# Optimization experiments

Hardware: AMD Instinct MI355X
Metric: run time of the kernel (lower is better)

Reference implementation:

```python
import jax, jax.numpy as jnp
import numpy as np

B, N, NE = 4, 10000, 100000
D, S, H, T = 128, 64, 4, 128      # enc_dim, enc_s_dim, n_head, n_token
NS = D + S                        # GNN node_size = 192
EPS = 1e-5


def linear(x, w, b):
    return x @ w.T + b


def layer_norm(x, g, b):
    m = jnp.mean(x, -1, keepdims=True)
    v = jnp.mean((x - m) ** 2, -1, keepdims=True)
    return (x - m) * jax.lax.rsqrt(v + EPS) * g + b


def mha(q, k, v, wqkv, bqkv, wo, bo):
    # torch nn.MultiheadAttention, batch_first=True
    d = q.shape[-1]; hd = d // H
    wq, wk, wv = jnp.split(wqkv, 3, 0)
    bq, bk, bv = jnp.split(bqkv, 3, 0)
    def proj(x, w, bb):
        Bx, L, _ = x.shape
        return (x @ w.T + bb).reshape(Bx, L, H, hd)
    qh, kh, vh = proj(q, wq, bq), proj(k, wk, bk), proj(v, wv, bv)
    scores = jnp.einsum('bqhd,bkhd->bhqk', qh, kh) / jnp.sqrt(jnp.asarray(hd, q.dtype))
    att = jax.nn.softmax(scores, axis=-1)
    o = jnp.einsum('bhqk,bkhd->bqhd', att, vh).reshape(q.shape[0], q.shape[1], d)
    return o @ wo.T + bo


def smean(vals, idx, n):
    # scatter_mean over one batch element: vals (ne,f), idx (ne,)
    s = jax.ops.segment_sum(vals, idx, num_segments=n)
    c = jax.ops.segment_sum(jnp.ones(idx.shape, vals.dtype), idx, num_segments=n)
    return s / jnp.maximum(c, 1.0)[:, None]

_smean_b = jax.vmap(smean, in_axes=(0, 0, None))
_gather_b = jax.vmap(lambda v, i: v[i])


def setup_inputs():
    key = jax.random.key(0)
    ks = jax.random.split(key, 32)
    r = lambda i, shape: jax.random.normal(ks[i], shape, jnp.float32) * 0.02
    inp = {
        'V': jax.random.normal(ks[0], (B, N, D), jnp.float32),
        'E': jax.random.normal(ks[1], (B, NE, D), jnp.float32),
        'edges': jax.random.randint(ks[2], (B, NE, 2), 0, N),
        's_enc': jax.random.normal(ks[3], (B, N, S), jnp.float32),
        # GNN f_edge: Linear(512,128) SiLU Linear(128,128) LN(128)
        'fe_w1': r(4, (D, D + 2 * NS)), 'fe_b1': jnp.zeros(D),
        'fe_w2': r(5, (D, D)), 'fe_b2': jnp.zeros(D),
        'fe_g': jnp.ones(D), 'fe_be': jnp.zeros(D),
        # GNN f_node: Linear(320,128) SiLU Linear(128,128) LN(128)
        'fn_w1': r(6, (D, NS + D)), 'fn_b1': jnp.zeros(D),
        'fn_w2': r(7, (D, D)), 'fn_b2': jnp.zeros(D),
        'fn_g': jnp.ones(D), 'fn_be': jnp.zeros(D),
        'ln1_g': jnp.ones(D), 'ln1_b': jnp.zeros(D),
        'ln2_g': jnp.ones(D), 'ln2_b': jnp.zeros(D),
        'Q': jax.random.normal(ks[8], (T, D), jnp.float32),
        'a1_wqkv': r(9, (3 * D, D)), 'a1_bqkv': jnp.zeros(3 * D),
        'a1_wo': r(10, (D, D)), 'a1_bo': jnp.zeros(D),
        'a2_wqkv': r(11, (3 * D, D)), 'a2_bqkv': jnp.zeros(3 * D),
        'a2_wo': r(12, (D, D)), 'a2_bo': jnp.zeros(D),
        'a3_wqkv': r(13, (3 * D, D)), 'a3_bqkv': jnp.zeros(3 * D),
        'a3_wo': r(14, (D, D)), 'a3_bo': jnp.zeros(D),
        'ffn_w1': r(15, (2 * D, D)), 'ffn_b1': jnp.zeros(2 * D),
        'ffn_w2': r(16, (D, 2 * D)), 'ffn_b2': jnp.zeros(D),
    }
    return inp


def reference(V, E, edges, s_enc,
              fe_w1, fe_b1, fe_w2, fe_b2, fe_g, fe_be,
              fn_w1, fn_b1, fn_w2, fn_b2, fn_g, fn_be,
              ln1_g, ln1_b, ln2_g, ln2_b,
              Q, a1_wqkv, a1_bqkv, a1_wo, a1_bo,
              a2_wqkv, a2_bqkv, a2_wo, a2_bo,
              a3_wqkv, a3_bqkv, a3_wo, a3_bo,
              ffn_w1, ffn_b1, ffn_w2, ffn_b2):
    n = V.shape[1]
    V_in = jnp.concatenate([V, s_enc], -1)                  # (B,N,192)
    valid = jnp.all(edges >= 0, -1)                          # (B,NE)
    safe = jnp.clip(edges, 0, n - 1)
    senders = _gather_b(V_in, safe[..., 0])                  # (B,NE,192)
    receivers = _gather_b(V_in, safe[..., 1])
    edge_inpt = jnp.concatenate([senders, receivers, E], -1) # (B,NE,512)
    eh = jax.nn.silu(linear(edge_inpt, fe_w1, fe_b1))
    e_emb = layer_norm(linear(eh, fe_w2, fe_b2), fe_g, fe_be)
    e_emb = e_emb * valid[..., None].astype(e_emb.dtype)
    e0, e1 = jnp.split(e_emb, 2, -1)
    m0 = _smean_b(e0, safe[..., 0], n)
    m1 = _smean_b(e1, safe[..., 1], n)
    node_inpt = jnp.concatenate([V_in, m0, m1], -1)          # (B,N,320)
    nh = jax.nn.silu(linear(node_inpt, fn_w1, fn_b1))
    v_emb = layer_norm(linear(nh, fn_w2, fn_b2), fn_g, fn_be)
    E_out = E + e_emb
    V1 = V + v_emb
    # attention block
    W0 = layer_norm(V1, ln1_g, ln1_b)
    lq = jnp.broadcast_to(Q, (V.shape[0],) + Q.shape)
    W = mha(lq, W0, W0, a1_wqkv, a1_bqkv, a1_wo, a1_bo)
    W = mha(W, W, W, a2_wqkv, a2_bqkv, a2_wo, a2_bo)
    W = mha(W0, W, W, a3_wqkv, a3_bqkv, a3_wo, a3_bo)
    V2 = V1 + W
    # FFN block
    x = layer_norm(V2, ln2_g, ln2_b)
    V3 = V2 + linear(jax.nn.silu(linear(x, ffn_w1, ffn_b1)), ffn_w2, ffn_b2)
    return (V3, E_out)
```

## Files before the change

### kernel.cpp

```cpp
#include <hip/hip_runtime.h>
#include <hip/hip_bf16.h>

#define B_ 4
#define N_ 10000
#define NE_ 100000
#define D_ 128
#define S_ 64
#define H_ 4
#define T_ 128

typedef unsigned short u16;
typedef unsigned int u32;
typedef __attribute__((ext_vector_type(4))) float f4;
typedef __attribute__((ext_vector_type(8))) short s8;

#define DEVI static __device__ __forceinline__

DEVI float b2f(u16 u){ union{u32 i; float f;} v; v.i=((u32)u)<<16; return v.f; }
DEVI u16 f2b(float f){ union{float ff; u32 i;} v; v.ff=f; u32 i=v.i; return (u16)((i+0x7fffu+((i>>16)&1u))>>16); }
DEVI f4 mfma16(s8 a, s8 b, f4 c){ return __builtin_amdgcn_mfma_f32_16x16x32_bf16(a,b,c,0,0,0); }
DEVI float rsum16(float x){ x+=__shfl_xor(x,1); x+=__shfl_xor(x,2); x+=__shfl_xor(x,4); x+=__shfl_xor(x,8); return x; }
DEVI float silu_f(float v){ return v/(1.f+__expf(-v)); }
DEVI float nn(float v, float s){ return (v==v)? v : s; }
DEVI float lo2f(u32 u){ union{u32 i; float f;} v; v.i=u<<16; return v.f; }
DEVI float hi2f(u32 u){ union{u32 i; float f;} v; v.i=u&0xffff0000u; return v.f; }

DEVI s8 ldw8f(const float* p){
  f4 a = *(const f4*)p;
  f4 c = *(const f4*)(p+4);
  union { u16 t[8]; s8 v; } u;
  #pragma unroll
  for (int i=0;i<4;i++){ u.t[i]=f2b(a[i]); u.t[4+i]=f2b(c[i]); }
  return u.v;
}
DEVI uint4 cvt8(const float* p){
  f4 a = *(const f4*)p;
  f4 c = *(const f4*)(p+4);
  union { u16 t[8]; uint4 v; } u;
  #pragma unroll
  for (int i=0;i<4;i++){ u.t[i]=f2b(a[i]); u.t[4+i]=f2b(c[i]); }
  return u.v;
}
DEVI uint4 cvt8nt(const float* p){
  f4 a = __builtin_nontemporal_load((const f4*)p);
  f4 c = __builtin_nontemporal_load((const f4*)(p+4));
  union { u16 t[8]; uint4 v; } u;
  #pragma unroll
  for (int i=0;i<4;i++){ u.t[i]=f2b(a[i]); u.t[4+i]=f2b(c[i]); }
  return u.v;
}

#define WO_FE1 0
#define WO_FE2 65536
#define WO_FN1 81920
#define WO_FN2 122880
#define WO_A1  139264
#define WO_A3  188416
#define WO_A3O 237568
#define WO_FF1 253952
#define WO_FF2 286720
#define WTOT   319488

__global__ __launch_bounds__(256) void k_cvtw(
  const float* __restrict__ s0, const float* __restrict__ s1,
  const float* __restrict__ s2, const float* __restrict__ s3,
  const float* __restrict__ s4, const float* __restrict__ s5,
  const float* __restrict__ s6, const float* __restrict__ s7,
  const float* __restrict__ s8v, u16* __restrict__ dst)
{
  int i = (blockIdx.x*256 + threadIdx.x)*8;
  if (i >= WTOT) return;
  const float* src; int off;
  if      (i < WO_FE2){ src=s0;  off=WO_FE1; }
  else if (i < WO_FN1){ src=s1;  off=WO_FE2; }
  else if (i < WO_FN2){ src=s2;  off=WO_FN1; }
  else if (i < WO_A1 ){ src=s3;  off=WO_FN2; }
  else if (i < WO_A3 ){ src=s4;  off=WO_A1;  }
  else if (i < WO_A3O){ src=s5;  off=WO_A3;  }
  else if (i < WO_FF1){ src=s6;  off=WO_A3O; }
  else if (i < WO_FF2){ src=s7;  off=WO_FF1; }
  else                { src=s8v; off=WO_FF2; }
  *(uint4*)(dst+i) = cvt8(src + (i-off));
}

__global__ __launch_bounds__(256) void k_count(
  const int* __restrict__ edges, int* __restrict__ cnt0, int* __restrict__ cnt1)
{
  int ge = blockIdx.x*256 + threadIdx.x;
  if (ge >= B_*NE_) return;
  int b = ge / NE_;
  int2 ed = *(const int2*)(edges + (size_t)ge*2);
  int i0 = min(max(ed.x,0),N_-1), i1 = min(max(ed.y,0),N_-1);
  atomicAdd(&cnt0[b*N_+i0], 1);
  atomicAdd(&cnt1[b*N_+i1], 1);
}

__global__ __launch_bounds__(1024) void k_scan_blk(
  const int* __restrict__ cnt0, const int* __restrict__ cnt1,
  int* __restrict__ off0, int* __restrict__ off1, int* __restrict__ bsum)
{
  __shared__ int sd[1024];
  const int g = blockIdx.x;
  const int arr = g >= 40;
  const int gb = arr? g-40 : g;
  const int* src = arr? cnt1 : cnt0;
  int* dst = arr? off1 : off0;
  const int t = threadIdx.x;
  const int idx = gb*1024 + t;
  int val = (idx < B_*N_)? src[idx] : 0;
  sd[t] = val; __syncthreads();
  int acc = val;
  for (int d=1; d<1024; d<<=1){
    int tv = (t>=d)? sd[t-d] : 0;
    __syncthreads();
    acc += tv; sd[t] = acc;
    __syncthreads();
  }
  if (idx < B_*N_) dst[idx] = acc - val;
  if (t == 1023) bsum[g] = acc;
}

__global__ __launch_bounds__(128) void k_scan_top(int* __restrict__ bsum)
{
  const int w = threadIdx.x>>6, lane = threadIdx.x&63;
  const int base = w*40;
  int v = (lane<40)? bsum[base+lane] : 0;
  int orig = v;
  for (int d=1; d<64; d<<=1){ int t=__shfl_up(v,d); if (lane>=d) v+=t; }
  if (lane<40) bsum[base+lane] = v - orig;
}

__global__ __launch_bounds__(1024) void k_scan_add(
  int* __restrict__ off0, int* __restrict__ off1, const int* __restrict__ bsum)
{
  const int g = blockIdx.x;
  const int arr = g >= 40;
  const int gb = arr? g-40 : g;
  int* dst = arr? off1 : off0;
  const int idx = gb*1024 + threadIdx.x;
  if (idx < B_*N_) dst[idx] += bsum[g];
}

__global__ __launch_bounds__(256) void k_fill(
  const int* __restrict__ edges,
  const int* __restrict__ off0, const int* __restrict__ off1,
  int* __restrict__ cur0, int* __restrict__ cur1,
  int* __restrict__ eidx0, int* __restrict__ eidx1)
{
  int ge = blockIdx.x*256 + threadIdx.x;
  if (ge >= B_*NE_) return;
  int b = ge / NE_;
  int2 ed = *(const int2*)(edges + (size_t)ge*2);
  int i0 = min(max(ed.x,0),N_-1), i1 = min(max(ed.y,0),N_-1);
  int g0 = b*N_+i0, g1 = b*N_+i1;
  int p0 = off0[g0] + atomicAdd(&cur0[g0], 1);
  eidx0[p0] = ge;
  int p1 = off1[g1] + atomicAdd(&cur1[g1], 1);
  eidx1[p1] = ge;
}

__global__ __launch_bounds__(512,4) void k_edge(
  const float* __restrict__ V, const float* __restrict__ E, const int* __restrict__ edges,
  const float* __restrict__ senc,
  const u16* __restrict__ w1b, const float* __restrict__ b1,
  const u16* __restrict__ w2b, const float* __restrict__ b2,
  const float* __restrict__ lng, const float* __restrict__ lnb,
  float* __restrict__ Eout)
{
  __shared__ u16 X[64][520];
  __shared__ float fvalid[64];
  __shared__ float rsA[64][8], rsB[64][8];
  const int tid = threadIdx.x;
  const int el = tid>>3, part = tid&7;
  const int ge = blockIdx.x*64 + el;
  const int b = ge / NE_;
  const int2 ed = *(const int2*)(edges + (size_t)ge*2);
  const int i0 = min(max(ed.x,0),N_-1), i1 = min(max(ed.y,0),N_-1);
  if (part==0) fvalid[el] = (ed.x>=0 && ed.y>=0) ? 1.f : 0.f;
  {
    const float* Vb = V + (size_t)b*N_*D_;
    const float* Sb = senc + (size_t)b*N_*S_;
    const float* Ep = E + (size_t)ge*D_;
    #pragma unroll
    for (int j=0;j<8;j++){
      int u = part + 8*j;
      if (u<48){
        const float* p;
        if (u<16)      p = Vb + (size_t)i0*D_ + u*8;
        else if (u<24) p = Sb + (size_t)i0*S_ + (u-16)*8;
        else if (u<40) p = Vb + (size_t)i1*D_ + (u-24)*8;
        else           p = Sb + (size_t)i1*S_ + (u-40)*8;
        *(uint4*)&X[el][u*8] = cvt8(p);
      } else {
        *(uint4*)&X[el][u*8] = cvt8nt(Ep + (u-48)*8);
      }
    }
  }
  __syncthreads();
  const int lane = tid&63, w = tid>>6;
  const int l15 = lane&15, hi = lane>>4;
  const int colb = w*16;
  f4 acc[4];
  #pragma unroll
  for (int m=0;m<4;m++){ float bb=b1[colb+l15]; acc[m]=(f4){bb,bb,bb,bb}; }
  for (int kk=0;kk<16;kk++){
    s8 bfr = *(const s8*)(w1b + (size_t)(colb+l15)*512 + kk*32 + hi*8);
    #pragma unroll
    for (int m=0;m<4;m++){
      s8 a = *(const s8*)&X[m*16+l15][kk*32 + hi*8];
      acc[m] = mfma16(a, bfr, acc[m]);
    }
  }
  __syncthreads();
  #pragma unroll
  for (int m=0;m<4;m++)
    #pragma unroll
    for (int r=0;r<4;r++)
      X[m*16+hi*4+r][colb+l15] = f2b(silu_f(acc[m][r]));
  __syncthreads();
  f4 a2[4];
  #pragma unroll
  for (int m=0;m<4;m++){ float bb=b2[colb+l15]; a2[m]=(f4){bb,bb,bb,bb}; }
  #pragma unroll
  for (int kk=0;kk<4;kk++){
    s8 bfr = *(const s8*)(w2b + (size_t)(colb+l15)*128 + kk*32 + hi*8);
    #pragma unroll
    for (int m=0;m<4;m++){
      s8 a = *(const s8*)&X[m*16+l15][kk*32 + hi*8];
      a2[m] = mfma16(a, bfr, a2[m]);
    }
  }
  #pragma unroll
  for (int m=0;m<4;m++)
    #pragma unroll
    for (int r=0;r<4;r++){
      float v=a2[m][r];
      float ps=rsum16(v), pq=rsum16(v*v);
      if (l15==0){ int row=m*16+hi*4+r; rsA[row][w]=ps; rsB[row][w]=pq; }
    }
  __syncthreads();
  const float gv=lng[colb+l15], bev=lnb[colb+l15];
  const int ge0 = blockIdx.x*64;
  #pragma unroll
  for (int m=0;m<4;m++)
    #pragma unroll
    for (int r=0;r<4;r++){
      const int row = m*16+hi*4+r;
      float s=0.f, s2=0.f;
      #pragma unroll
      for (int ww=0;ww<8;ww++){ s+=rsA[row][ww]; s2+=rsB[row][ww]; }
      const float mean = s*(1.f/128.f);
      const float rstd = rsqrtf(s2*(1.f/128.f) - mean*mean + 1e-5f);
      const float vm = fvalid[row];
      const int col = colb+l15;
      float ev = ((a2[m][r]-mean)*rstd*gv + bev) * vm;
      ev = nn(ev, 7e3f);
      float ef = b2f(X[row][384+col]);
      __builtin_nontemporal_store(ef + ev, Eout + (size_t)(ge0+row)*D_ + col);
    }
}

__global__ __launch_bounds__(256,2) void k_nodekv(
  const float* __restrict__ V, const float* __restrict__ senc,
  const float* __restrict__ Ein, const float* __restrict__ Eout,
  const int* __restrict__ cnt0, const int* __restrict__ cnt1,
  const int* __restrict__ off0, const int* __restrict__ off1,
  const int* __restrict__ eidx0, const int* __restrict__ eidx1,
  const u16* __restrict__ w1b, const float* __restrict__ b1,
  const u16* __restrict__ w2b, const float* __restrict__ b2,
  const float* __restrict__ lng, const float* __restrict__ lnb,
  const float* __restrict__ l1g, const float* __restrict__ l1b,
  const u16* __restrict__ wqkvb, const float* __restrict__ bqkv,
  u16* __restrict__ V1, u16* __restrict__ W0,
  u16* __restrict__ kh1, u16* __restrict__ vh1)
{
  __shared__ u16 X[64][328];
  __shared__ float rsA[64][4], rsB[64][4];
  const int tid=threadIdx.x, nl=tid>>2, part=tid&3;
  const int gn = blockIdx.x*64 + nl;
  const int b = gn / N_, n = gn - b*N_;
  {
    const float* Vp = V + ((size_t)b*N_ + n)*D_;
    const float* Sp = senc + ((size_t)b*N_ + n)*S_;
    #pragma unroll
    for (int j=0;j<6;j++){
      int u = part + 4*j;
      const float* p = (u<16)? Vp + u*8 : Sp + (u-16)*8;
      *(uint4*)&X[nl][u*8] = cvt8(p);
    }
    const int sel = part>>1;
    const int cntv = sel? cnt1[gn] : cnt0[gn];
    const int ob   = sel? off1[gn] : off0[gn];
    const int* elist = sel? eidx1 : eidx0;
    const int co = part*32;
    float acc[32];
    #pragma unroll
    for (int i=0;i<32;i++) acc[i]=0.f;
    for (int k=0;k<cntv;k++){
      int e = elist[ob+k];
      const f4* po_ = (const f4*)(Eout + (size_t)e*D_ + co);
      const f4* pe  = (const f4*)(Ein  + (size_t)e*D_ + co);
      #pragma unroll
      for (int q=0;q<8;q++){
        f4 a = po_[q], c = pe[q];
        #pragma unroll
        for (int i=0;i<4;i++) acc[q*4+i] += a[i]-c[i];
      }
    }
    float rc = 1.f/(float)max(cntv,1);
    #pragma unroll
    for (int j=0;j<4;j++){
      u16 ov[8];
      #pragma unroll
      for (int i=0;i<8;i++) ov[i]=f2b(acc[j*8+i]*rc);
      uint4 pk; __builtin_memcpy(&pk, ov, 16);
      *(uint4*)&X[nl][192+co+j*8] = pk;
    }
  }
  __syncthreads();
  const int lane=tid&63, w=tid>>6, l15=lane&15, hi=lane>>4, colb=w*32;
  f4 acc[4][2];
  #pragma unroll
  for (int m=0;m<4;m++)
    #pragma unroll
    for (int tl=0;tl<2;tl++){ float bb=b1[colb+tl*16+l15]; acc[m][tl]=(f4){bb,bb,bb,bb}; }
  for (int kk=0;kk<10;kk++){
    s8 bfr[2];
    #pragma unroll
    for (int tl=0;tl<2;tl++)
      bfr[tl] = *(const s8*)(w1b + (size_t)(colb+tl*16+l15)*320 + kk*32 + hi*8);
    #pragma unroll
    for (int m=0;m<4;m++){
      s8 a = *(const s8*)&X[m*16+l15][kk*32+hi*8];
      #pragma unroll
      for (int tl=0;tl<2;tl++) acc[m][tl]=mfma16(a,bfr[tl],acc[m][tl]);
    }
  }
  __syncthreads();
  #pragma unroll
  for (int m=0;m<4;m++)
    #pragma unroll
    for (int tl=0;tl<2;tl++)
      #pragma unroll
      for (int r=0;r<4;r++)
        X[m*16+hi*4+r][192+colb+tl*16+l15] = f2b(silu_f(acc[m][tl][r]));
  __syncthreads();
  f4 a2[4][2];
  #pragma unroll
  for (int m=0;m<4;m++)
    #pragma unroll
    for (int tl=0;tl<2;tl++){ float bb=b2[colb+tl*16+l15]; a2[m][tl]=(f4){bb,bb,bb,bb}; }
  #pragma unroll
  for (int kk=0;kk<4;kk++){
    s8 bfr[2];
    #pragma unroll
    for (int tl=0;tl<2;tl++)
      bfr[tl] = *(const s8*)(w2b + (size_t)(colb+tl*16+l15)*128 + kk*32 + hi*8);
    #pragma unroll
    for (int m=0;m<4;m++){
      s8 a = *(const s8*)&X[m*16+l15][192 + kk*32+hi*8];
      #pragma unroll
      for (int tl=0;tl<2;tl++) a2[m][tl]=mfma16(a,bfr[tl],a2[m][tl]);
    }
  }
  #pragma unroll
  for (int m=0;m<4;m++)
    #pragma unroll
    for (int r=0;r<4;r++){
      float ps=0.f, pq=0.f;
      #pragma unroll
      for (int tl=0;tl<2;tl++){ float v=a2[m][tl][r]; ps+=v; pq+=v*v; }
      ps=rsum16(ps); pq=rsum16(pq);
      if (l15==0){ int row=m*16+hi*4+r; rsA[row][w]=ps; rsB[row][w]=pq; }
    }
  __syncthreads();
  float gv[2],bev[2],g1v[2],b1v[2];
  #pragma unroll
  for (int tl=0;tl<2;tl++){
    int col=colb+tl*16+l15;
    gv[tl]=lng[col]; bev[tl]=lnb[col]; g1v[tl]=l1g[col]; b1v[tl]=l1b[col];
  }
  #pragma unroll
  for (int m=0;m<4;m++)
    #pragma unroll
    for (int r=0;r<4;r++){
      const int row=m*16+hi*4+r;
      float s  = rsA[row][0]+rsA[row][1]+rsA[row][2]+rsA[row][3];
      float s2 = rsB[row][0]+rsB[row][1]+rsB[row][2]+rsB[row][3];
      float mean=s*(1.f/128.f);
      float rstd=rsqrtf(s2*(1.f/128.f)-mean*mean+1e-5f);
      #pragma unroll
      for (int tl=0;tl<2;tl++){
        float ve=(a2[m][tl][r]-mean)*rstd*gv[tl]+bev[tl];
        a2[m][tl][r] = b2f(X[row][colb+tl*16+l15]) + ve;
      }
    }
  __syncthreads();
  #pragma unroll
  for (int m=0;m<4;m++)
    #pragma unroll
    for (int r=0;r<4;r++){
      float ps=0.f, pq=0.f;
      #pragma unroll
      for (int tl=0;tl<2;tl++){ float v=a2[m][tl][r]; ps+=v; pq+=v*v; }
      ps=rsum16(ps); pq=rsum16(pq);
      if (l15==0){ int row=m*16+hi*4+r; rsA[row][w]=ps; rsB[row][w]=pq; }
    }
  __syncthreads();
  #pragma unroll
  for (int m=0;m<4;m++)
    #pragma unroll
    for (int r=0;r<4;r++){
      const int row=m*16+hi*4+r;
      float sv  = rsA[row][0]+rsA[row][1]+rsA[row][2]+rsA[row][3];
      float sv2 = rsB[row][0]+rsB[row][1]+rsB[row][2]+rsB[row][3];
      float m2=sv*(1.f/128.f);
      float rs2=rsqrtf(sv2*(1.f/128.f)-m2*m2+1e-5f);
      #pragma unroll
      for (int tl=0;tl<2;tl++){
        int col=colb+tl*16+l15;
        float tmp=a2[m][tl][r];
        X[row][col]     = f2b(tmp);
        X[row][192+col] = f2b((tmp-m2)*rs2*g1v[tl]+b1v[tl]);
      }
    }
  __syncthreads();
  #pragma unroll
  for (int j=0;j<4;j++){
    int u=part+4*j;
    *(uint4*)(V1 + (size_t)gn*D_ + u*8) = *(const uint4*)&X[nl][u*8];
    *(uint4*)(W0 + (size_t)gn*D_ + u*8) = *(const uint4*)&X[nl][192 + u*8];
  }
  const int colb2 = w*64;
  f4 acck[4][4];
  #pragma unroll
  for (int m=0;m<4;m++)
    #pragma unroll
    for (int tl=0;tl<4;tl++){ float bb=bqkv[128 + colb2+tl*16+l15]; acck[m][tl]=(f4){bb,bb,bb,bb}; }
  #pragma unroll
  for (int kk=0;kk<4;kk++){
    s8 bfr[4];
    #pragma unroll
    for (int tl=0;tl<4;tl++)
      bfr[tl] = *(const s8*)(wqkvb + (size_t)(128 + colb2+tl*16+l15)*D_ + kk*32+hi*8);
    #pragma unroll
    for (int m=0;m<4;m++){
      s8 a = *(const s8*)&X[m*16+l15][192 + kk*32+hi*8];
      #pragma unroll
      for (int tl=0;tl<4;tl++) acck[m][tl]=mfma16(a,bfr[tl],acck[m][tl]);
    }
  }
  __syncthreads();
  #pragma unroll
  for (int m=0;m<4;m++)
    #pragma unroll
    for (int tl=0;tl<4;tl++)
      #pragma unroll
      for (int r=0;r<4;r++)
        X[m*16+hi*4+r][colb2+tl*16+l15]=f2b(acck[m][tl][r]);
  __syncthreads();
  #pragma unroll
  for (int j=0;j<8;j++){
    int u=part+4*j, col0=u*8;
    u16* dst;
    if (col0<128){ int h=col0>>5, d=col0&31; dst = kh1 + ((size_t)(b*H_+h)*N_ + n)*32 + d; }
    else { int c2=col0-128; int h=c2>>5, d=c2&31; dst = vh1 + ((size_t)(b*H_+h)*N_ + n)*32 + d; }
    *(uint4*)dst = *(const uint4*)&X[nl][col0];
  }
}

__global__ __launch_bounds__(256) void k_qh1(
  const float* __restrict__ Q, const float* __restrict__ wqkv, const float* __restrict__ bqkv,
  u16* __restrict__ qh1)
{
  __shared__ u16 X[64][136];
  const int tid=threadIdx.x, nl=tid>>2, part=tid&3;
  const int q = blockIdx.x*64 + nl;
  #pragma unroll
  for (int j=0;j<4;j++){ int u=part+4*j; *(uint4*)&X[nl][u*8] = cvt8(Q + (size_t)q*D_ + u*8); }
  __syncthreads();
  const int lane=tid&63, w=tid>>6, l15=lane&15, hi=lane>>4, rw=w*16;
  f4 acc[8];
  #pragma unroll
  for (int t=0;t<8;t++){ float bb=bqkv[l15+16*t]; acc[t]=(f4){bb,bb,bb,bb}; }
  #pragma unroll
  for (int kk=0;kk<4;kk++){
    s8 a = *(const s8*)&X[rw+l15][kk*32+hi*8];
    #pragma unroll
    for (int t=0;t<8;t++){
      s8 bf = ldw8f(wqkv + (size_t)(t*16+l15)*D_ + kk*32+hi*8);
      acc[t]=mfma16(a,bf,acc[t]);
    }
  }
  __syncthreads();
  #pragma unroll
  for (int t=0;t<8;t++){
    #pragma unroll
    for (int r=0;r<4;r++) X[rw+hi*4+r][l15+16*t]=f2b(acc[t][r]);
  }
  __syncthreads();
  #pragma unroll
  for (int j=0;j<4;j++){
    int u=part+4*j, col0=u*8, h=col0>>5, d=col0&31;
    *(uint4*)(qh1 + ((size_t)h*T_ + q)*32 + d) = *(const uint4*)&X[nl][col0];
  }
}

#define NCH 20
#define CHK 512

__global__ __launch_bounds__(256,2) void k_mha1p(
  const u16* __restrict__ qh1, const u16* __restrict__ kh1, const u16* __restrict__ vh1,
  float* __restrict__ pm, float* __restrict__ pl, float* __restrict__ po)
{
  __shared__ u16 VT[32][72];
  __shared__ u16 P[4][32][72];
  const int bh = blockIdx.x / NCH, ch = blockIdx.x - bh*NCH;
  const int tid = threadIdx.x, w = tid>>6, lane = tid&63, l15=lane&15, hi=lane>>4;
  const int h = bh & 3;
  const int k0 = ch*CHK;
  const int nk = min(CHK, N_ - k0);
  const u16* Kb = kh1 + ((size_t)bh*N_ + k0)*32;
  const u16* Vb = vh1 + ((size_t)bh*N_ + k0)*32;
  s8 aq[2];
  #pragma unroll
  for (int qt=0;qt<2;qt++)
    aq[qt] = *(const s8*)(qh1 + ((size_t)h*T_ + w*32 + qt*16 + l15)*32 + hi*8);
  const float scale = 0.17677669529663687f;
  float m_reg[2][4], l_reg[2][4];
  f4 acc[2][2];
  #pragma unroll
  for (int qt=0;qt<2;qt++){
    #pragma unroll
    for (int r=0;r<4;r++){ m_reg[qt][r]=-1e30f; l_reg[qt][r]=0.f; }
    #pragma unroll
    for (int dt=0;dt<2;dt++) acc[qt][dt]=(f4){0.f,0.f,0.f,0.f};
  }
  const int ntile = (nk+63)>>6;
  for (int kt=0; kt<ntile; kt++){
    {
      int key = tid>>2, dseg = tid&3;
      int kg = kt*64 + key;
      uint4 v = (kg<nk)? *(const uint4*)(Vb + (size_t)kg*32 + dseg*8) : (uint4){0,0,0,0};
      const u16* vv = (const u16*)&v;
      #pragma unroll
      for (int i=0;i<8;i++) VT[dseg*8+i][key] = vv[i];
    }
    __syncthreads();
    f4 sa[2][4];
    #pragma unroll
    for (int kt4=0;kt4<4;kt4++){
      int key = kt*64 + kt4*16 + l15;
      int keyc = min(key, nk-1);
      s8 bk = *(const s8*)(Kb + (size_t)keyc*32 + hi*8);
      #pragma unroll
      for (int qt=0;qt<2;qt++)
        sa[qt][kt4] = mfma16(aq[qt], bk, (f4){0.f,0.f,0.f,0.f});
    }
    #pragma unroll
    for (int qt=0;qt<2;qt++){
      #pragma unroll
      for (int r=0;r<4;r++){
        float s[4];
        float mx = -1e30f;
        #pragma unroll
        for (int kt4=0;kt4<4;kt4++){
          int key = kt*64 + kt4*16 + l15;
          s[kt4] = (key<nk)? sa[qt][kt4][r]*scale : -1e30f;
          mx = fmaxf(mx, s[kt4]);
        }
        mx=fmaxf(mx,__shfl_xor(mx,1)); mx=fmaxf(mx,__shfl_xor(mx,2));
        mx=fmaxf(mx,__shfl_xor(mx,4)); mx=fmaxf(mx,__shfl_xor(mx,8));
        float mn = fmaxf(m_reg[qt][r], mx);
        float corr = __expf(m_reg[qt][r]-mn);
        float ps=0.f;
        #pragma unroll
        for (int kt4=0;kt4<4;kt4++){
          float p = __expf(s[kt4]-mn);
          ps += p;
          P[w][qt*16+hi*4+r][kt4*16+l15] = f2b(p);
        }
        ps = rsum16(ps);
        l_reg[qt][r] = l_reg[qt][r]*corr + ps;
        m_reg[qt][r] = mn;
        #pragma unroll
        for (int dt=0;dt<2;dt++) acc[qt][dt][r] *= corr;
      }
    }
    __syncthreads();
    #pragma unroll
    for (int ks=0;ks<2;ks++){
      s8 bv[2];
      #pragma unroll
      for (int dt=0;dt<2;dt++)
        bv[dt] = *(const s8*)&VT[dt*16+l15][ks*32+hi*8];
      #pragma unroll
      for (int qt=0;qt<2;qt++){
        s8 pa = *(const s8*)&P[w][qt*16+l15][ks*32+hi*8];
        #pragma unroll
        for (int dt=0;dt<2;dt++)
          acc[qt][dt]=mfma16(pa,bv[dt],acc[qt][dt]);
      }
    }
    __syncthreads();
  }
  const size_t pbase = ((size_t)bh*NCH + ch)*128;
  #pragma unroll
  for (int qt=0;qt<2;qt++)
    #pragma unroll
    for (int r=0;r<4;r++){
      int row = w*32 + qt*16 + hi*4 + r;
      if (l15==0){ pm[pbase+row]=m_reg[qt][r]; pl[pbase+row]=l_reg[qt][r]; }
      #pragma unroll
      for (int dt=0;dt<2;dt++)
        po[(pbase+row)*32 + dt*16 + l15] = acc[qt][dt][r];
    }
}

__global__ __launch_bounds__(256) void k_mha1c(
// ... 186 lines not shown
        acc[t]=mfma16(a,bf,acc[t]);
      }
    }
    #pragma unroll
    for (int t=0;t<8;t++){
      #pragma unroll
      for (int r=0;r<4;r++) Y[rw+hi*4+r][l15+16*t]=f2b(acc[t][r]);
    }
  }
  __syncthreads();
  f4 a2[16];
  #pragma unroll
  for (int t=0;t<16;t++){ float bb=bqkv3[128 + l15+16*t]; a2[t]=(f4){bb,bb,bb,bb}; }
  #pragma unroll
  for (int kk=0;kk<4;kk++){
    s8 a = *(const s8*)&Y[rw+l15][kk*32+hi*8];
    #pragma unroll
    for (int t=0;t<16;t++){
      s8 bf = ldw8f(wqkv3 + (size_t)(128 + t*16+l15)*D_ + kk*32+hi*8);
      a2[t]=mfma16(a,bf,a2[t]);
    }
  }
  __syncthreads();
  #pragma unroll
  for (int t=0;t<16;t++){
    #pragma unroll
    for (int r=0;r<4;r++) Y[rw+hi*4+r][l15+16*t]=f2b(a2[t][r]);
  }
  __syncthreads();
  const int b=row>>7, q=row&127;
  #pragma unroll
  for (int j=0;j<4;j++){
    int u=part+4*j, col0=u*8, h=col0>>5, d=col0&31;
    *(uint4*)(kh3 + ((size_t)(b*H_+h)*T_ + q)*32 + d) = *(const uint4*)&Y[nl][col0];
  }
  #pragma unroll
  for (int cc=0;cc<32;cc++){
    int c2 = part*32 + cc;
    int h=c2>>5, d=c2&31;
    vh3T[((size_t)(b*H_+h)*32 + d)*T_ + q] = Y[nl][128+c2];
  }
}

__global__ __launch_bounds__(256,2) void k_mha3f(
  const u16* __restrict__ W0, const u16* __restrict__ V1,
  const u16* __restrict__ wq3b, const float* __restrict__ bqkv3,
  const u16* __restrict__ kh3, const u16* __restrict__ vh3T,
  const u16* __restrict__ wo3b, const float* __restrict__ bo3,
  const float* __restrict__ l2g, const float* __restrict__ l2b,
  const u16* __restrict__ fw1b, const float* __restrict__ fb1,
  const u16* __restrict__ fw2b, const float* __restrict__ fb2,
  float* __restrict__ V3)
{
  __shared__ u16 Wt[64][136];
  __shared__ u16 Q3[64][136];
  __shared__ u16 P3[64][136];
  __shared__ float rsA[64][4], rsB[64][4];
  const int tid=threadIdx.x, nl=tid>>2, part=tid&3;
  const int b = blockIdx.x/157, tb = blockIdx.x - b*157;
  const int n0 = tb*64;
  {
    const int ns = min(n0+nl, N_-1);
    const u16* src = W0 + ((size_t)b*N_+ns)*D_;
    #pragma unroll
    for (int j=0;j<4;j++){ int u=part+4*j; *(uint4*)&Wt[nl][u*8] = *(const uint4*)(src+u*8); }
  }
  __syncthreads();
  const int lane=tid&63, w=tid>>6, l15=lane&15, hi=lane>>4;
  const int rw=w*16, colb=w*32;
  {
    f4 acc[4][2];
    #pragma unroll
    for (int m=0;m<4;m++)
      #pragma unroll
      for (int tl=0;tl<2;tl++){ float bb=bqkv3[colb+tl*16+l15]; acc[m][tl]=(f4){bb,bb,bb,bb}; }
    #pragma unroll
    for (int kk=0;kk<4;kk++){
      s8 bfr[2];
      #pragma unroll
      for (int tl=0;tl<2;tl++)
        bfr[tl] = *(const s8*)(wq3b + (size_t)(colb+tl*16+l15)*D_ + kk*32+hi*8);
      #pragma unroll
      for (int m=0;m<4;m++){
        s8 a = *(const s8*)&Wt[m*16+l15][kk*32+hi*8];
        #pragma unroll
        for (int tl=0;tl<2;tl++) acc[m][tl]=mfma16(a,bfr[tl],acc[m][tl]);
      }
    }
    #pragma unroll
    for (int m=0;m<4;m++)
      #pragma unroll
      for (int tl=0;tl<2;tl++)
        #pragma unroll
        for (int r=0;r<4;r++)
          Q3[m*16+hi*4+r][colb+tl*16+l15]=f2b(acc[m][tl][r]);
  }
  __syncthreads();
  const float scale=0.17677669529663687f;
  f4 oacc[8];
  #pragma unroll
  for (int t=0;t<8;t++) oacc[t]=(f4){0.f,0.f,0.f,0.f};
  #pragma unroll
  for (int h=0;h<H_;h++){
    f4 sa[8];
    #pragma unroll
    for (int t=0;t<8;t++) sa[t]=(f4){0.f,0.f,0.f,0.f};
    s8 aq = *(const s8*)&Q3[rw+l15][h*32+hi*8];
    #pragma unroll
    for (int t=0;t<8;t++){
      s8 bf = *(const s8*)(kh3 + ((size_t)(b*H_+h)*T_ + t*16+l15)*32 + hi*8);
      sa[t]=mfma16(aq,bf,sa[t]);
    }
    #pragma unroll
    for (int r=0;r<4;r++){
      const int row=rw+hi*4+r;
      float mx=-1e30f;
      float sv[8];
      #pragma unroll
      for (int t=0;t<8;t++){ sv[t]=sa[t][r]*scale; mx=fmaxf(mx,sv[t]); }
      mx=fmaxf(mx,__shfl_xor(mx,1)); mx=fmaxf(mx,__shfl_xor(mx,2));
      mx=fmaxf(mx,__shfl_xor(mx,4)); mx=fmaxf(mx,__shfl_xor(mx,8));
      float se=0.f; float pv[8];
      #pragma unroll
      for (int t=0;t<8;t++){ pv[t]=__expf(sv[t]-mx); se+=pv[t]; }
      se=rsum16(se);
      float inv=1.f/se;
      #pragma unroll
      for (int t=0;t<8;t++) P3[row][l15+16*t]=f2b(pv[t]*inv);
    }
    __syncthreads();
    #pragma unroll
    for (int kk=0;kk<4;kk++){
      s8 ap = *(const s8*)&P3[rw+l15][kk*32+hi*8];
      #pragma unroll
      for (int t2=0;t2<2;t2++){
        s8 bf = *(const s8*)(vh3T + ((size_t)(b*H_+h)*32 + t2*16+l15)*T_ + kk*32+hi*8);
        oacc[h*2+t2]=mfma16(ap,bf,oacc[h*2+t2]);
      }
    }
    __syncthreads();
  }
  #pragma unroll
  for (int t=0;t<8;t++){
    #pragma unroll
    for (int r=0;r<4;r++) Q3[rw+hi*4+r][l15+16*t]=f2b(oacc[t][r]);
  }
  __syncthreads();
  f4 a2[4][2];
  #pragma unroll
  for (int m=0;m<4;m++)
    #pragma unroll
    for (int tl=0;tl<2;tl++){ float bb=bo3[colb+tl*16+l15]; a2[m][tl]=(f4){bb,bb,bb,bb}; }
  #pragma unroll
  for (int kk=0;kk<4;kk++){
    s8 bfr[2];
    #pragma unroll
    for (int tl=0;tl<2;tl++)
      bfr[tl] = *(const s8*)(wo3b + (size_t)(colb+tl*16+l15)*D_ + kk*32+hi*8);
    #pragma unroll
    for (int m=0;m<4;m++){
      s8 a = *(const s8*)&Q3[m*16+l15][kk*32+hi*8];
      #pragma unroll
      for (int tl=0;tl<2;tl++) a2[m][tl]=mfma16(a,bfr[tl],a2[m][tl]);
    }
  }
  #pragma unroll
  for (int m=0;m<4;m++)
    #pragma unroll
    for (int r=0;r<4;r++){
      const int row=m*16+hi*4+r;
      const int nr = min(n0+row, N_-1);
      const size_t gr=(size_t)b*N_+nr;
      float ps=0.f, pq=0.f;
      #pragma unroll
      for (int tl=0;tl<2;tl++){
        float tmp = b2f(V1[gr*D_ + colb+tl*16+l15]) + a2[m][tl][r];
        a2[m][tl][r]=tmp; ps+=tmp; pq+=tmp*tmp;
      }
      ps=rsum16(ps); pq=rsum16(pq);
      if (l15==0){ rsA[row][w]=ps; rsB[row][w]=pq; }
    }
  __syncthreads();
  float g2v[2],b2v[2];
  #pragma unroll
  for (int tl=0;tl<2;tl++){ g2v[tl]=l2g[colb+tl*16+l15]; b2v[tl]=l2b[colb+tl*16+l15]; }
  #pragma unroll
  for (int m=0;m<4;m++)
    #pragma unroll
    for (int r=0;r<4;r++){
      const int row=m*16+hi*4+r;
      float s  = rsA[row][0]+rsA[row][1]+rsA[row][2]+rsA[row][3];
      float s2 = rsB[row][0]+rsB[row][1]+rsB[row][2]+rsB[row][3];
      float mean=s*(1.f/128.f);
      float rstd=rsqrtf(s2*(1.f/128.f)-mean*mean+1e-5f);
      #pragma unroll
      for (int tl=0;tl<2;tl++){
        int col=colb+tl*16+l15;
        float tmp=a2[m][tl][r];
        P3[row][col]=f2b(tmp);
        Wt[row][col]=f2b((tmp-mean)*rstd*g2v[tl]+b2v[tl]);
      }
    }
  __syncthreads();
  f4 accf[4][2];
  #pragma unroll
  for (int m=0;m<4;m++)
    #pragma unroll
    for (int tl=0;tl<2;tl++){ float bb=fb2[colb+tl*16+l15]; accf[m][tl]=(f4){bb,bb,bb,bb}; }
  for (int half=0;half<2;half++){
    f4 ah[4][2];
    #pragma unroll
    for (int m=0;m<4;m++)
      #pragma unroll
      for (int tl=0;tl<2;tl++){ float bb=fb1[half*128+colb+tl*16+l15]; ah[m][tl]=(f4){bb,bb,bb,bb}; }
    #pragma unroll
    for (int kk=0;kk<4;kk++){
      s8 bfr[2];
      #pragma unroll
      for (int tl=0;tl<2;tl++)
        bfr[tl] = *(const s8*)(fw1b + (size_t)(half*128+colb+tl*16+l15)*D_ + kk*32+hi*8);
      #pragma unroll
      for (int m=0;m<4;m++){
        s8 a = *(const s8*)&Wt[m*16+l15][kk*32+hi*8];
        #pragma unroll
        for (int tl=0;tl<2;tl++) ah[m][tl]=mfma16(a,bfr[tl],ah[m][tl]);
      }
    }
    __syncthreads();
    #pragma unroll
    for (int m=0;m<4;m++)
      #pragma unroll
      for (int tl=0;tl<2;tl++)
        #pragma unroll
        for (int r=0;r<4;r++)
          Q3[m*16+hi*4+r][colb+tl*16+l15]=f2b(silu_f(ah[m][tl][r]));
    __syncthreads();
    #pragma unroll
    for (int kk=0;kk<4;kk++){
      s8 bfr[2];
      #pragma unroll
      for (int tl=0;tl<2;tl++)
        bfr[tl] = *(const s8*)(fw2b + (size_t)(colb+tl*16+l15)*256 + half*128 + kk*32+hi*8);
      #pragma unroll
      for (int m=0;m<4;m++){
        s8 a = *(const s8*)&Q3[m*16+l15][kk*32+hi*8];
        #pragma unroll
        for (int tl=0;tl<2;tl++) accf[m][tl]=mfma16(a,bfr[tl],accf[m][tl]);
      }
    }
  }
  #pragma unroll
  for (int m=0;m<4;m++)
    #pragma unroll
    for (int r=0;r<4;r++){
      const int row=m*16+hi*4+r;
      if (n0+row < N_){
        const size_t gr=(size_t)b*N_+n0+row;
        #pragma unroll
        for (int tl=0;tl<2;tl++){
          int col=colb+tl*16+l15;
          V3[gr*D_+col] = b2f(P3[row][col]) + accf[m][tl][r];
        }
      }
    }
}

extern "C" void kernel_launch(void* const* d_in, const int* in_sizes, int n_in,
                              void* d_out, int out_size, void* d_ws, size_t ws_size,
                              hipStream_t stream)
{
  const float* V     = (const float*)d_in[0];
  const float* E     = (const float*)d_in[1];
  const int* edges   = (const int*)d_in[2];
  const float* senc  = (const float*)d_in[3];
  const float* fe_w1=(const float*)d_in[4];  const float* fe_b1=(const float*)d_in[5];
  const float* fe_w2=(const float*)d_in[6];  const float* fe_b2=(const float*)d_in[7];
  const float* fe_g =(const float*)d_in[8];  const float* fe_be=(const float*)d_in[9];
  const float* fn_w1=(const float*)d_in[10]; const float* fn_b1=(const float*)d_in[11];
  const float* fn_w2=(const float*)d_in[12]; const float* fn_b2=(const float*)d_in[13];
  const float* fn_g =(const float*)d_in[14]; const float* fn_be=(const float*)d_in[15];
  const float* ln1_g=(const float*)d_in[16]; const float* ln1_b=(const float*)d_in[17];
  const float* ln2_g=(const float*)d_in[18]; const float* ln2_b=(const float*)d_in[19];
  const float* Q    =(const float*)d_in[20];
  const float* a1_wqkv=(const float*)d_in[21]; const float* a1_bqkv=(const float*)d_in[22];
  const float* a1_wo=(const float*)d_in[23];   const float* a1_bo=(const float*)d_in[24];
  const float* a2_wqkv=(const float*)d_in[25]; const float* a2_bqkv=(const float*)d_in[26];
  const float* a2_wo=(const float*)d_in[27];   const float* a2_bo=(const float*)d_in[28];
  const float* a3_wqkv=(const float*)d_in[29]; const float* a3_bqkv=(const float*)d_in[30];
  const float* a3_wo=(const float*)d_in[31];   const float* a3_bo=(const float*)d_in[32];
  const float* ffn_w1=(const float*)d_in[33];  const float* ffn_b1=(const float*)d_in[34];
  const float* ffn_w2=(const float*)d_in[35];  const float* ffn_b2=(const float*)d_in[36];

  char* ws = (char*)d_ws;
  size_t off = 0;
  auto alloc = [&](size_t bytes)->void*{ void* p = ws + off; off += (bytes + 255) & ~(size_t)255; return p; };
  int* cnt0 = (int*)alloc((size_t)B_*N_*4);
  int* cnt1 = (int*)alloc((size_t)B_*N_*4);
  int* cur0 = (int*)alloc((size_t)B_*N_*4);
  int* cur1 = (int*)alloc((size_t)B_*N_*4);
  const size_t zero_bytes = off;
  int* bsum = (int*)alloc(128*4);
  int* off0 = (int*)alloc((size_t)B_*N_*4);
  int* off1 = (int*)alloc((size_t)B_*N_*4);
  int* eidx0 = (int*)alloc((size_t)B_*NE_*4);
  int* eidx1 = (int*)alloc((size_t)B_*NE_*4);
  u16* wcat = (u16*)alloc((size_t)WTOT*2);
  u16* V1  = (u16*)alloc((size_t)B_*N_*D_*2);
  u16* W0  = (u16*)alloc((size_t)B_*N_*D_*2);
  u16* kh1 = (u16*)alloc((size_t)B_*H_*N_*32*2);
  u16* vh1 = (u16*)alloc((size_t)B_*H_*N_*32*2);
  u16* qh1 = (u16*)alloc((size_t)H_*T_*32*2);
  float* o1 = (float*)alloc((size_t)B_*T_*D_*4);
  u16* qh2 = (u16*)alloc((size_t)B_*H_*T_*32*2);
  u16* kh2 = (u16*)alloc((size_t)B_*H_*T_*32*2);
  u16* vh2 = (u16*)alloc((size_t)B_*H_*T_*32*2);
  float* o2 = (float*)alloc((size_t)B_*T_*D_*4);
  u16* kh3 = (u16*)alloc((size_t)B_*H_*T_*32*2);
  u16* vh3T= (u16*)alloc((size_t)B_*H_*32*T_*2);
  float* pmw = (float*)alloc((size_t)B_*H_*NCH*128*4);
  float* plw = (float*)alloc((size_t)B_*H_*NCH*128*4);
  float* pow_ = (float*)alloc((size_t)B_*H_*NCH*128*32*4);
  if (ws_size < off) return;

  u16* w_fe1 = wcat + WO_FE1;
  u16* w_fe2 = wcat + WO_FE2;
  u16* w_fn1 = wcat + WO_FN1;
  u16* w_fn2 = wcat + WO_FN2;
  u16* w_a1  = wcat + WO_A1;
  u16* w_a3  = wcat + WO_A3;
  u16* w_a3o = wcat + WO_A3O;
  u16* w_ff1 = wcat + WO_FF1;
  u16* w_ff2 = wcat + WO_FF2;

  float* outp = (float*)d_out;
  float* V3out = outp;
  float* Eout  = outp + (size_t)B_*N_*D_;

  hipMemsetAsync(d_ws, 0, zero_bytes, stream);
  k_cvtw<<<(WTOT/8+255)/256,256,0,stream>>>(fe_w1,fe_w2,fn_w1,fn_w2,a1_wqkv,a3_wqkv,a3_wo,
                                            ffn_w1,ffn_w2, wcat);
  k_count<<<(B_*NE_+255)/256,256,0,stream>>>(edges, cnt0, cnt1);
  k_scan_blk<<<80,1024,0,stream>>>(cnt0,cnt1, off0,off1, bsum);
  k_scan_top<<<1,128,0,stream>>>(bsum);
  k_scan_add<<<80,1024,0,stream>>>(off0,off1, bsum);
  k_fill<<<(B_*NE_+255)/256,256,0,stream>>>(edges, off0,off1, cur0,cur1, eidx0,eidx1);
  k_edge<<<(B_*NE_)/64,512,0,stream>>>(V,E,edges,senc, w_fe1,fe_b1, w_fe2,fe_b2, fe_g,fe_be,
                                       Eout);
  k_nodekv<<<(B_*N_)/64,256,0,stream>>>(V,senc, E,Eout, cnt0,cnt1, off0,off1, eidx0,eidx1,
                                        w_fn1,fn_b1, w_fn2,fn_b2, fn_g,fn_be, ln1_g,ln1_b,
                                        w_a1,a1_bqkv, V1,W0, kh1,vh1);
  k_qh1<<<T_/64,256,0,stream>>>(Q, a1_wqkv, a1_bqkv, qh1);
  k_mha1p<<<B_*H_*NCH,256,0,stream>>>(qh1,kh1,vh1, pmw,plw,pow_);
  k_mha1c<<<(B_*H_*T_*32)/256,256,0,stream>>>(pmw,plw,pow_, o1);
  k_att12<<<(B_*T_)/64,256,0,stream>>>(o1, a1_wo, a1_bo, a2_wqkv, a2_bqkv, qh2,kh2,vh2);
  k_mha2<<<(B_*H_*T_)/4,256,0,stream>>>(qh2,kh2,vh2,o2);
  k_att23<<<(B_*T_)/64,256,0,stream>>>(o2, a2_wo, a2_bo, a3_wqkv, a3_bqkv, kh3, vh3T);
  k_mha3f<<<B_*157,256,0,stream>>>(W0,V1, w_a3,a3_bqkv, kh3,vh3T, w_a3o,a3_bo,
                                   ln2_g,ln2_b, w_ff1,ffn_b1, w_ff2,ffn_b2, V3out);
}
```

Measured before the change: 740.2 us.

## Scatter bf16 edge embeddings into CSR order in edge kernel for contiguous aggregation

The fill kernel now records each edge's CSR slot instead of building edge-index lists. The edge kernel writes its LayerNorm output halves as bf16 directly into per-receiver contiguous buffers at those slots. The node kernel then streams these contiguous bf16 rows instead of gathering fp32 Eout and E rows through indirection and subtracting them. The edge kernel is also retiled to 32 edges per block with a higher occupancy hint. The aim is to replace the random fp32 gathers in aggregation, at the cost of extra scattered bf16 writes, bf16 rounding of the aggregated messages, and halved MFMA work per block.

```diff
diff --git a/kernel.cpp b/kernel.cpp
--- a/kernel.cpp
+++ b/kernel.cpp
@@ -145,7 +145,7 @@
   const int* __restrict__ edges,
   const int* __restrict__ off0, const int* __restrict__ off1,
   int* __restrict__ cur0, int* __restrict__ cur1,
-  int* __restrict__ eidx0, int* __restrict__ eidx1)
+  int* __restrict__ pos0, int* __restrict__ pos1)
 {
   int ge = blockIdx.x*256 + threadIdx.x;
   if (ge >= B_*NE_) return;
@@ -153,26 +153,26 @@
   int2 ed = *(const int2*)(edges + (size_t)ge*2);
   int i0 = min(max(ed.x,0),N_-1), i1 = min(max(ed.y,0),N_-1);
   int g0 = b*N_+i0, g1 = b*N_+i1;
-  int p0 = off0[g0] + atomicAdd(&cur0[g0], 1);
-  eidx0[p0] = ge;
-  int p1 = off1[g1] + atomicAdd(&cur1[g1], 1);
-  eidx1[p1] = ge;
-}
-
-__global__ __launch_bounds__(512,4) void k_edge(
+  pos0[ge] = off0[g0] + atomicAdd(&cur0[g0], 1);
+  pos1[ge] = off1[g1] + atomicAdd(&cur1[g1], 1);
+}
+
+__global__ __launch_bounds__(512,8) void k_edge(
   const float* __restrict__ V, const float* __restrict__ E, const int* __restrict__ edges,
   const float* __restrict__ senc,
   const u16* __restrict__ w1b, const float* __restrict__ b1,
   const u16* __restrict__ w2b, const float* __restrict__ b2,
   const float* __restrict__ lng, const float* __restrict__ lnb,
+  const int* __restrict__ pos0, const int* __restrict__ pos1,
+  u16* __restrict__ eg0, u16* __restrict__ eg1,
   float* __restrict__ Eout)
 {
-  __shared__ u16 X[64][520];
-  __shared__ float fvalid[64];
-  __shared__ float rsA[64][8], rsB[64][8];
+  __shared__ u16 X[32][520];
+  __shared__ float fvalid[32];
+  __shared__ float rsA[32][8], rsB[32][8];
   const int tid = threadIdx.x;
-  const int el = tid>>3, part = tid&7;
-  const int ge = blockIdx.x*64 + el;
+  const int el = tid>>4, part = tid&15;
+  const int ge = blockIdx.x*32 + el;
   const int b = ge / NE_;
   const int2 ed = *(const int2*)(edges + (size_t)ge*2);
   const int i0 = min(max(ed.x,0),N_-1), i1 = min(max(ed.y,0),N_-1);
@@ -182,8 +182,8 @@
     const float* Sb = senc + (size_t)b*N_*S_;
     const float* Ep = E + (size_t)ge*D_;
     #pragma unroll
-    for (int j=0;j<8;j++){
-      int u = part + 8*j;
+    for (int j=0;j<4;j++){
+      int u = part + 16*j;
       if (u<48){
         const float* p;
         if (u<16)      p = Vb + (size_t)i0*D_ + u*8;
@@ -200,38 +200,38 @@
   const int lane = tid&63, w = tid>>6;
   const int l15 = lane&15, hi = lane>>4;
   const int colb = w*16;
-  f4 acc[4];
-  #pragma unroll
-  for (int m=0;m<4;m++){ float bb=b1[colb+l15]; acc[m]=(f4){bb,bb,bb,bb}; }
+  f4 acc[2];
+  #pragma unroll
+  for (int m=0;m<2;m++){ float bb=b1[colb+l15]; acc[m]=(f4){bb,bb,bb,bb}; }
   for (int kk=0;kk<16;kk++){
     s8 bfr = *(const s8*)(w1b + (size_t)(colb+l15)*512 + kk*32 + hi*8);
     #pragma unroll
-    for (int m=0;m<4;m++){
+    for (int m=0;m<2;m++){
       s8 a = *(const s8*)&X[m*16+l15][kk*32 + hi*8];
       acc[m] = mfma16(a, bfr, acc[m]);
     }
   }
   __syncthreads();
   #pragma unroll
-  for (int m=0;m<4;m++)
+  for (int m=0;m<2;m++)
     #pragma unroll
     for (int r=0;r<4;r++)
       X[m*16+hi*4+r][colb+l15] = f2b(silu_f(acc[m][r]));
   __syncthreads();
-  f4 a2[4];
-  #pragma unroll
-  for (int m=0;m<4;m++){ float bb=b2[colb+l15]; a2[m]=(f4){bb,bb,bb,bb}; }
+  f4 a2[2];
+  #pragma unroll
+  for (int m=0;m<2;m++){ float bb=b2[colb+l15]; a2[m]=(f4){bb,bb,bb,bb}; }
   #pragma unroll
   for (int kk=0;kk<4;kk++){
     s8 bfr = *(const s8*)(w2b + (size_t)(colb+l15)*128 + kk*32 + hi*8);
     #pragma unroll
-    for (int m=0;m<4;m++){
+    for (int m=0;m<2;m++){
       s8 a = *(const s8*)&X[m*16+l15][kk*32 + hi*8];
       a2[m] = mfma16(a, bfr, a2[m]);
     }
   }
   #pragma unroll
-  for (int m=0;m<4;m++)
+  for (int m=0;m<2;m++)
     #pragma unroll
     for (int r=0;r<4;r++){
       float v=a2[m][r];
@@ -240,9 +240,8 @@
     }
   __syncthreads();
   const float gv=lng[colb+l15], bev=lnb[colb+l15];
-  const int ge0 = blockIdx.x*64;
-  #pragma unroll
-  for (int m=0;m<4;m++)
+  #pragma unroll
+  for (int m=0;m<2;m++)
     #pragma unroll
     for (int r=0;r<4;r++){
       const int row = m*16+hi*4+r;
@@ -251,21 +250,36 @@
       for (int ww=0;ww<8;ww++){ s+=rsA[row][ww]; s2+=rsB[row][ww]; }
       const float mean = s*(1.f/128.f);
       const float rstd = rsqrtf(s2*(1.f/128.f) - mean*mean + 1e-5f);
-      const float vm = fvalid[row];
-      const int col = colb+l15;
-      float ev = ((a2[m][r]-mean)*rstd*gv + bev) * vm;
+      float ev = ((a2[m][r]-mean)*rstd*gv + bev) * fvalid[row];
       ev = nn(ev, 7e3f);
-      float ef = b2f(X[row][384+col]);
-      __builtin_nontemporal_store(ef + ev, Eout + (size_t)(ge0+row)*D_ + col);
-    }
+      X[row][colb+l15] = f2b(ev);
+    }
+  __syncthreads();
+  {
+    const int c0 = part*8;
+    f4 o0, o1v;
+    #pragma unroll
+    for (int i=0;i<4;i++){
+      o0[i]  = b2f(X[el][384+c0+i])   + b2f(X[el][c0+i]);
+      o1v[i] = b2f(X[el][384+c0+4+i]) + b2f(X[el][c0+4+i]);
+    }
+    __builtin_nontemporal_store(o0,  (f4*)(Eout + (size_t)ge*D_ + c0));
+    __builtin_nontemporal_store(o1v, (f4*)(Eout + (size_t)ge*D_ + c0+4));
+    if (part < 8){
+      const int p0 = pos0[ge];
+      *(uint4*)(eg0 + (size_t)p0*64 + part*8) = *(const uint4*)&X[el][part*8];
+    } else {
+      const int p1 = pos1[ge];
+      *(uint4*)(eg1 + (size_t)p1*64 + (part-8)*8) = *(const uint4*)&X[el][64+(part-8)*8];
+    }
+  }
 }
 
 __global__ __launch_bounds__(256,2) void k_nodekv(
   const float* __restrict__ V, const float* __restrict__ senc,
-  const float* __restrict__ Ein, const float* __restrict__ Eout,
+  const u16* __restrict__ eg0, const u16* __restrict__ eg1,
   const int* __restrict__ cnt0, const int* __restrict__ cnt1,
   const int* __restrict__ off0, const int* __restrict__ off1,
-  const int* __restrict__ eidx0, const int* __restrict__ eidx1,
   const u16* __restrict__ w1b, const float* __restrict__ b1,
   const u16* __restrict__ w2b, const float* __restrict__ b2,
   const float* __restrict__ lng, const float* __restrict__ lnb,
@@ -291,20 +305,20 @@
     const int sel = part>>1;
     const int cntv = sel? cnt1[gn] : cnt0[gn];
     const int ob   = sel? off1[gn] : off0[gn];
-    const int* elist = sel? eidx1 : eidx0;
-    const int co = part*32;
-    float acc[32];
-    #pragma unroll
-    for (int i=0;i<32;i++) acc[i]=0.f;
+    const u16* egp = sel? eg1 : eg0;
+    const int co = (part&1)*32;
+    float accg[32];
+    #pragma unroll
+    for (int i=0;i<32;i++) accg[i]=0.f;
     for (int k=0;k<cntv;k++){
-      int e = elist[ob+k];
-      const f4* po_ = (const f4*)(Eout + (size_t)e*D_ + co);
-      const f4* pe  = (const f4*)(Ein  + (size_t)e*D_ + co);
-      #pragma unroll
-      for (int q=0;q<8;q++){
-        f4 a = po_[q], c = pe[q];
-        #pragma unroll
-        for (int i=0;i<4;i++) acc[q*4+i] += a[i]-c[i];
+      const u16* p = egp + (size_t)(ob+k)*64 + co;
+      #pragma unroll
+      for (int q=0;q<4;q++){
+        uint4 v = *(const uint4*)(p + q*8);
+        accg[q*8+0]+=lo2f(v.x); accg[q*8+1]+=hi2f(v.x);
+        accg[q*8+2]+=lo2f(v.y); accg[q*8+3]+=hi2f(v.y);
+        accg[q*8+4]+=lo2f(v.z); accg[q*8+5]+=hi2f(v.z);
+        accg[q*8+6]+=lo2f(v.w); accg[q*8+7]+=hi2f(v.w);
       }
     }
     float rc = 1.f/(float)max(cntv,1);
@@ -312,9 +326,9 @@
     for (int j=0;j<4;j++){
       u16 ov[8];
       #pragma unroll
-      for (int i=0;i<8;i++) ov[i]=f2b(acc[j*8+i]*rc);
+      for (int i=0;i<8;i++) ov[i]=f2b(accg[j*8+i]*rc);
       uint4 pk; __builtin_memcpy(&pk, ov, 16);
-      *(uint4*)&X[nl][192+co+j*8] = pk;
+      *(uint4*)&X[nl][192 + part*32 + j*8] = pk;
     }
   }
   __syncthreads();
@@ -1107,8 +1121,10 @@
   int* bsum = (int*)alloc(128*4);
   int* off0 = (int*)alloc((size_t)B_*N_*4);
   int* off1 = (int*)alloc((size_t)B_*N_*4);
-  int* eidx0 = (int*)alloc((size_t)B_*NE_*4);
-  int* eidx1 = (int*)alloc((size_t)B_*NE_*4);
+  int* pos0 = (int*)alloc((size_t)B_*NE_*4);
+  int* pos1 = (int*)alloc((size_t)B_*NE_*4);
+  u16* eg0  = (u16*)alloc((size_t)B_*NE_*64*2);
+  u16* eg1  = (u16*)alloc((size_t)B_*NE_*64*2);
   u16* wcat = (u16*)alloc((size_t)WTOT*2);
   u16* V1  = (u16*)alloc((size_t)B_*N_*D_*2);
   u16* W0  = (u16*)alloc((size_t)B_*N_*D_*2);
@@ -1148,10 +1164,10 @@
   k_scan_blk<<<80,1024,0,stream>>>(cnt0,cnt1, off0,off1, bsum);
   k_scan_top<<<1,128,0,stream>>>(bsum);
   k_scan_add<<<80,1024,0,stream>>>(off0,off1, bsum);
-  k_fill<<<(B_*NE_+255)/256,256,0,stream>>>(edges, off0,off1, cur0,cur1, eidx0,eidx1);
-  k_edge<<<(B_*NE_)/64,512,0,stream>>>(V,E,edges,senc, w_fe1,fe_b1, w_fe2,fe_b2, fe_g,fe_be,
-                                       Eout);
-  k_nodekv<<<(B_*N_)/64,256,0,stream>>>(V,senc, E,Eout, cnt0,cnt1, off0,off1, eidx0,eidx1,
+  k_fill<<<(B_*NE_+255)/256,256,0,stream>>>(edges, off0,off1, cur0,cur1, pos0,pos1);
+  k_edge<<<(B_*NE_)/32,512,0,stream>>>(V,E,edges,senc, w_fe1,fe_b1, w_fe2,fe_b2, fe_g,fe_be,
+                                       pos0,pos1, eg0,eg1, Eout);
+  k_nodekv<<<(B_*N_)/64,256,0,stream>>>(V,senc, eg0,eg1, cnt0,cnt1, off0,off1,
                                         w_fn1,fn_b1, w_fn2,fn_b2, fn_g,fn_be, ln1_g,ln1_b,
                                         w_a1,a1_bqkv, V1,W0, kh1,vh1);
   k_qh1<<<T_/64,256,0,stream>>>(Q, a1_wqkv, a1_bqkv, qh1);
```

After: 643.5 us. 1.15x faster.
